# Optimization experiments

Measured on AMD Instinct MI355X. Metric: run time of the kernel, lower is better.

## Reference

```python
import jax, jax.numpy as jnp
import numpy as np

N_HEAD = 16
N_FEAT = 1024
D_K = N_FEAT // N_HEAD


def setup_inputs() -> dict:
    key = jax.random.key(0)
    ks = jax.random.split(key, 11)
    B, T1, T2 = 2, 2048, 2048
    s = 0.02
    return {
        "query": jax.random.normal(ks[0], (B, T1, N_FEAT), jnp.float32),
        "key_": jax.random.normal(ks[1], (B, T2, N_FEAT), jnp.float32),
        "value": jax.random.normal(ks[2], (B, T2, N_FEAT), jnp.float32),
        "mask": jnp.ones((B, T1, T2), jnp.int32),
        "Wq": jax.random.normal(ks[3], (N_FEAT, N_FEAT), jnp.float32) * s,
        "bq": jnp.zeros((N_FEAT,), jnp.float32),
        "Wk": jax.random.normal(ks[4], (N_FEAT, N_FEAT), jnp.float32) * s,
        "bk": jnp.zeros((N_FEAT,), jnp.float32),
        "Wv": jax.random.normal(ks[5], (N_FEAT, N_FEAT), jnp.float32) * s,
        "bv": jnp.zeros((N_FEAT,), jnp.float32),
        "Wo": jax.random.normal(ks[6], (N_FEAT, N_FEAT), jnp.float32) * s,
        "bo": jnp.zeros((N_FEAT,), jnp.float32),
    }


def reference(query, key_, value, mask, Wq, bq, Wk, bk, Wv, bv, Wo, bo):
    B = query.shape[0]
    # project and split heads: (B, T, F) -> (B, H, T, d_k)
    def heads(x, W, b):
        y = x @ W + b
        return y.reshape(B, -1, N_HEAD, D_K).transpose(0, 2, 1, 3)

    q = heads(query, Wq, bq)
    k = heads(key_, Wk, bk)
    v = heads(value, Wv, bv)

    scale = jnp.sqrt(jnp.asarray(D_K, jnp.float32))
    scores = jnp.einsum("bhqd,bhkd->bhqk", q, k) / scale  # (B,H,T1,T2)
    m = mask[:, None, :, :]  # (B,1,T1,T2)
    scores = jnp.where(m > 0, scores, jnp.asarray(-10000.0, scores.dtype))
    attn = jax.nn.softmax(scores, axis=-1)
    # dropout_rate = 0.0 / inference -> identity
    x = jnp.einsum("bhqk,bhkd->bhqd", attn, v)
    x = x.transpose(0, 2, 1, 3).reshape(B, -1, N_FEAT)
    return x @ Wo + bo
```

## Files before the change

### kernel.cpp

```cpp
#include <hip/hip_runtime.h>
#include <hip/hip_bf16.h>
#include <stdint.h>

typedef float  f32x4 __attribute__((ext_vector_type(4)));
typedef short  s16x8 __attribute__((ext_vector_type(8)));
typedef short  s16x4 __attribute__((ext_vector_type(4)));
typedef int    i32x4 __attribute__((ext_vector_type(4)));

#define DI __device__ __forceinline__

constexpr int Bb = 2, Tt = 2048, Ff = 1024, Hh = 16, Dk = 64;
constexpr int Mm = Bb * Tt;
constexpr float LOG2E = 1.44269504088896340736f;

DI ushort f2bf(float f) {
  unsigned u = __float_as_uint(f);
  unsigned r = (u + 0x7fffu + ((u >> 16) & 1u)) >> 16;
  return (ushort)r;
}

DI int cvt_pk_bf16(float lo, float hi) {
  __hip_bfloat162 t = __float22bfloat162_rn(make_float2(lo, hi));
  int w;
  __builtin_memcpy(&w, &t, 4);
  return w;
}

DI void gload16(const void* g, void* l) {
  __builtin_amdgcn_global_load_lds(
      (__attribute__((address_space(1))) void*)g,
      (__attribute__((address_space(3))) void*)l, 16, 0, 0);
}

__global__ __launch_bounds__(256) void cvt3_kernel(const float* __restrict__ s0, const float* __restrict__ s1,
                                                   const float* __restrict__ s2, ushort* __restrict__ d0,
                                                   ushort* __restrict__ d1, ushort* __restrict__ d2, int n8) {
  const float* src = blockIdx.y == 0 ? s0 : (blockIdx.y == 1 ? s1 : s2);
  ushort* dst = blockIdx.y == 0 ? d0 : (blockIdx.y == 1 ? d1 : d2);
  int i = blockIdx.x * 256 + threadIdx.x;
  if (i >= n8) return;
  const float4* s4 = (const float4*)src + (size_t)i * 2;
  float4 a = s4[0], b = s4[1];
  s16x8 o;
  o[0] = (short)f2bf(a.x); o[1] = (short)f2bf(a.y); o[2] = (short)f2bf(a.z); o[3] = (short)f2bf(a.w);
  o[4] = (short)f2bf(b.x); o[5] = (short)f2bf(b.y); o[6] = (short)f2bf(b.z); o[7] = (short)f2bf(b.w);
  *((s16x8*)dst + i) = o;
}

__global__ __launch_bounds__(256) void wtrans_kernel(const float* __restrict__ W0, const float* __restrict__ W1,
                                                     const float* __restrict__ W2, const float* __restrict__ W3,
                                                     ushort* __restrict__ Wt0, ushort* __restrict__ Wt1,
                                                     ushort* __restrict__ Wt2, ushort* __restrict__ Wt3) {
  const float* W; ushort* Wt;
  switch (blockIdx.z) {
    case 0: W = W0; Wt = Wt0; break;
    case 1: W = W1; Wt = Wt1; break;
    case 2: W = W2; Wt = Wt2; break;
    default: W = W3; Wt = Wt3; break;
  }
  __shared__ float tile[64][65];
  int k0 = blockIdx.y * 64, n0 = blockIdx.x * 64;
  int t = threadIdx.x, r = t >> 4, c4 = (t & 15) * 4;
#pragma unroll
  for (int i = 0; i < 4; i++) {
    int row = r + i * 16;
    const float4 v = *(const float4*)(W + (size_t)(k0 + row) * Ff + n0 + c4);
    tile[row][c4] = v.x; tile[row][c4 + 1] = v.y; tile[row][c4 + 2] = v.z; tile[row][c4 + 3] = v.w;
  }
  __syncthreads();
#pragma unroll
  for (int i = 0; i < 4; i++) {
    int n = r + i * 16;
    s16x4 o;
#pragma unroll
    for (int j = 0; j < 4; j++) o[j] = (short)f2bf(tile[c4 + j][n]);
    *(s16x4*)(Wt + (size_t)(n0 + n) * Ff + k0 + c4) = o;
  }
}

__global__ __launch_bounds__(256) void maskflag_kernel(const int* __restrict__ mask, int* __restrict__ flags) {
  int kb = blockIdx.x, qb = blockIdx.y, b = blockIdx.z;
  int t = threadIdx.x;
  __shared__ int s;
  if (t == 0) s = 1;
  __syncthreads();
  int ok = 1;
#pragma unroll
  for (int i = 0; i < 4; i++) {
    int row = qb * 64 + (t >> 4) + i * 16;
    const int4 v = *(const int4*)(mask + ((size_t)b * Tt + row) * Tt + kb * 64 + (t & 15) * 4);
    ok &= (v.x > 0) & (v.y > 0) & (v.z > 0) & (v.w > 0);
  }
  atomicAnd(&s, ok);
  __syncthreads();
  if (t == 0) flags[(b * 32 + qb) * 32 + kb] = s;
}

DI void gemm_core(const ushort* __restrict__ A, const ushort* __restrict__ Bt,
                  const float* __restrict__ bias, void* __restrict__ Cout, float scale, int mode,
                  int m0, int n0) {
  __shared__ ushort Ads[2][128 * 64];
  __shared__ ushort Bds[2][128 * 64];
  const int tid = threadIdx.x, lane = tid & 63, w = tid >> 6;
  const int wr = w >> 1, wc = w & 1;
  const int g = lane >> 4, ln = lane & 15;
  const int srow = lane >> 3;
  const int swzch = ((lane & 7) ^ srow) * 8;

  f32x4 acc[4][4];
#pragma unroll
  for (int m = 0; m < 4; m++)
#pragma unroll
    for (int n = 0; n < 4; n++) acc[m][n] = (f32x4){0.f, 0.f, 0.f, 0.f};

#pragma unroll
  for (int it = 0; it < 4; ++it) {
    const int row = w * 32 + it * 8;
    gload16(A + (size_t)(m0 + row + srow) * Ff + swzch, Ads[0] + row * 64);
    gload16(Bt + (size_t)(n0 + row + srow) * Ff + swzch, Bds[0] + row * 64);
  }
  __syncthreads();

  for (int kk = 0; kk < 16; ++kk) {
    const int cur = kk & 1;
    const int k0 = kk * 64;
    if (kk < 15) {
#pragma unroll
      for (int it = 0; it < 4; ++it) {
        const int row = w * 32 + it * 8;
        gload16(A + (size_t)(m0 + row + srow) * Ff + k0 + 64 + swzch, Ads[cur ^ 1] + row * 64);
        gload16(Bt + (size_t)(n0 + row + srow) * Ff + k0 + 64 + swzch, Bds[cur ^ 1] + row * 64);
      }
    }
    s16x8 af[4][2], bf[4][2];
#pragma unroll
    for (int m = 0; m < 4; m++)
#pragma unroll
      for (int c = 0; c < 2; c++) {
        const int ra = wr * 64 + m * 16 + ln;
        const int off = (c * 64 + g * 16) ^ ((ra & 7) << 4);
        af[m][c] = *(const s16x8*)((const char*)(Ads[cur]) + ra * 128 + off);
      }
#pragma unroll
    for (int n = 0; n < 4; n++)
#pragma unroll
      for (int c = 0; c < 2; c++) {
        const int rb = wc * 64 + n * 16 + ln;
        const int off = (c * 64 + g * 16) ^ ((rb & 7) << 4);
        bf[n][c] = *(const s16x8*)((const char*)(Bds[cur]) + rb * 128 + off);
      }
#pragma unroll
    for (int m = 0; m < 4; m++)
#pragma unroll
      for (int n = 0; n < 4; n++)
#pragma unroll
        for (int c = 0; c < 2; c++)
          acc[m][n] = __builtin_amdgcn_mfma_f32_16x16x32_bf16(af[m][c], bf[n][c], acc[m][n], 0, 0, 0);
    if (kk < 15) __syncthreads();
  }
#pragma unroll
  for (int m = 0; m < 4; m++) {
    const int r0 = m0 + wr * 64 + m * 16 + g * 4;
#pragma unroll
    for (int n = 0; n < 4; n++) {
      const int col = n0 + wc * 64 + n * 16 + ln;
      const float bv = bias[col];
      if (mode == 2) {
        const int bb = r0 >> 11, rb = r0 & 2047;
        const int x = rb & 63;
        const int pbase = (x & 0x20) | ((x & 0x0C) << 1) | ((x & 0x10) >> 2);
        s16x4 o4;
#pragma unroll
        for (int r = 0; r < 4; r++) o4[r] = (short)f2bf(acc[m][n][r] + bv);
        *(s16x4*)((ushort*)Cout + ((size_t)bb * Ff + col) * Tt + (rb & ~63) + pbase) = o4;
      } else {
#pragma unroll
        for (int r = 0; r < 4; r++) {
          const float val = (acc[m][n][r] + bv) * scale;
          if (mode == 1)
            ((ushort*)Cout)[(size_t)(r0 + r) * Ff + col] = f2bf(val);
          else
            ((float*)Cout)[(size_t)(r0 + r) * Ff + col] = val;
        }
      }
    }
  }
}

__global__ __launch_bounds__(256) void qkv_gemm_kernel(
    const ushort* __restrict__ Xq, const ushort* __restrict__ Xk, const ushort* __restrict__ Xv,
    const ushort* __restrict__ Wqt, const ushort* __restrict__ Wkt, const ushort* __restrict__ Wvt,
    const float* __restrict__ bq, const float* __restrict__ bk, const float* __restrict__ bv,
    ushort* __restrict__ Qb, ushort* __restrict__ Kb, ushort* __restrict__ Vpt) {
  const int lin = blockIdx.x + 8 * blockIdx.y + 256 * blockIdx.z;
  const int work = (lin & 7) * 96 + (lin >> 3);
  const int z = work >> 8;
  const int r = work & 255;
  const int m0 = (r >> 3) * 128, n0 = (r & 7) * 128;
  const ushort* A = z == 0 ? Xq : (z == 1 ? Xk : Xv);
  const ushort* Wt = z == 0 ? Wqt : (z == 1 ? Wkt : Wvt);
  const float* bias = z == 0 ? bq : (z == 1 ? bk : bv);
  void* C = z == 0 ? (void*)Qb : (z == 1 ? (void*)Kb : (void*)Vpt);
  const float scale = z == 0 ? 0.125f * LOG2E : 1.0f;
  gemm_core(A, Wt, bias, C, scale, z == 2 ? 2 : 1, m0, n0);
}

__global__ __launch_bounds__(256) void out_gemm_kernel(const ushort* __restrict__ AO,
                                                       const ushort* __restrict__ Wot,
                                                       const float* __restrict__ bo,
                                                       float* __restrict__ Out) {
  const int lin = blockIdx.x + 8 * blockIdx.y;
  const int work = (lin & 7) * 32 + (lin >> 3);
  const int m0 = (work >> 3) * 128, n0 = (work & 7) * 128;
  gemm_core(AO, Wot, bo, Out, 1.0f, 0, m0, n0);
}

__global__ __launch_bounds__(256) void flash_kernel(
    const ushort* __restrict__ Qb, const ushort* __restrict__ Kb, const ushort* __restrict__ Vpt,
    const int* __restrict__ flags, const int* __restrict__ mask, ushort* __restrict__ AO) {
  __shared__ ushort Ks[2][64 * 64];
  __shared__ ushort Vs[2][64 * 64];
  const int lin = blockIdx.x + 16 * (blockIdx.y + 16 * blockIdx.z);
  const int work = (lin & 7) * 64 + (lin >> 3);
  const int qb = work & 15, h = (work >> 4) & 15, b = work >> 8;
  const int tid = threadIdx.x, lane = tid & 63, w = tid >> 6;
  const int g = lane >> 4, ln = lane & 15;

  const ushort* Qg = Qb + ((size_t)b * Tt + qb * 128) * Ff + h * Dk;
  const ushort* Kg = Kb + ((size_t)b * Tt) * Ff + h * Dk;
  const ushort* Vg = Vpt + (size_t)(b * Ff + h * Dk) * Tt;

  const int srow = lane >> 3;
  const int swzch = ((lane & 7) ^ srow) * 8;

#pragma unroll
  for (int it = 0; it < 2; ++it) {
    const int row = w * 16 + it * 8;
    gload16(Kg + (size_t)(row + srow) * Ff + swzch, Ks[0] + row * 64);
    gload16(Vg + (size_t)(row + srow) * Tt + swzch, Vs[0] + row * 64);
  }
  const int* flagrow0 = flags + (b * 32 + qb * 2) * 32;
  const int f0 = (lane < 32) ? flagrow0[lane] : 1;
  const int f1 = (lane < 32) ? flagrow0[32 + lane] : 1;

  s16x8 qf0[2], qf1[2];
  {
    const ushort* Qrow0 = Qg + (size_t)(w * 16 + ln) * Ff;
    const ushort* Qrow1 = Qrow0 + (size_t)64 * Ff;
    qf0[0] = *(const s16x8*)(Qrow0 + g * 8);
    qf0[1] = *(const s16x8*)(Qrow0 + 32 + g * 8);
    qf1[0] = *(const s16x8*)(Qrow1 + g * 8);
    qf1[1] = *(const s16x8*)(Qrow1 + 32 + g * 8);
  }
  __syncthreads();
  const unsigned long long bm0 = __ballot(f0 == 0);
  const unsigned long long bm1 = __ballot(f1 == 0);

  float l0 = 0.f, l1 = 0.f;
  f32x4 o0[4], o1[4];
#pragma unroll
  for (int ds = 0; ds < 4; ds++) { o0[ds] = (f32x4){0.f, 0.f, 0.f, 0.f}; o1[ds] = (f32x4){0.f, 0.f, 0.f, 0.f}; }

  auto body = [&](const ushort* Kc, const ushort* Vc, ushort* Kn, ushort* Vn, int kt) {
    if (kt + 1 < 32) {
      const ushort* Kg2 = Kg + (size_t)(kt + 1) * 64 * Ff;
      const ushort* Vg2 = Vg + (size_t)(kt + 1) * 64;
#pragma unroll
      for (int it = 0; it < 2; ++it) {
        const int row = w * 16 + it * 8;
        gload16(Kg2 + (size_t)(row + srow) * Ff + swzch, Kn + row * 64);
        gload16(Vg2 + (size_t)(row + srow) * Tt + swzch, Vn + row * 64);
      }
    }
    f32x4 sf0[4], sf1[4];
    __builtin_amdgcn_s_setprio(1);
#pragma unroll
    for (int ks = 0; ks < 4; ++ks) {
      f32x4 a0 = (f32x4){0.f, 0.f, 0.f, 0.f};
      f32x4 a1 = (f32x4){0.f, 0.f, 0.f, 0.f};
#pragma unroll
      for (int c = 0; c < 2; c++) {
        const int row = ks * 16 + ln;
        const int off = (c * 64 + g * 16) ^ ((row & 7) << 4);
        const s16x8 kf = *(const s16x8*)((const char*)Kc + row * 128 + off);
        a0 = __builtin_amdgcn_mfma_f32_16x16x32_bf16(kf, qf0[c], a0, 0, 0, 0);
        a1 = __builtin_amdgcn_mfma_f32_16x16x32_bf16(kf, qf1[c], a1, 0, 0, 0);
      }
      sf0[ks] = a0; sf1[ks] = a1;
    }
    __builtin_amdgcn_s_setprio(0);
    if ((bm0 >> kt) & 1ull) {
      const int qg_ = qb * 128 + w * 16 + ln;
#pragma unroll
      for (int ks = 0; ks < 4; ++ks) {
        const int4 mv = *(const int4*)(mask + ((size_t)b * Tt + qg_) * Tt + kt * 64 + ks * 16 + g * 4);
        if (mv.x <= 0) sf0[ks][0] = -10000.f;
        if (mv.y <= 0) sf0[ks][1] = -10000.f;
        if (mv.z <= 0) sf0[ks][2] = -10000.f;
        if (mv.w <= 0) sf0[ks][3] = -10000.f;
      }
    }
    if ((bm1 >> kt) & 1ull) {
      const int qg_ = qb * 128 + 64 + w * 16 + ln;
#pragma unroll
      for (int ks = 0; ks < 4; ++ks) {
        const int4 mv = *(const int4*)(mask + ((size_t)b * Tt + qg_) * Tt + kt * 64 + ks * 16 + g * 4);
        if (mv.x <= 0) sf1[ks][0] = -10000.f;
        if (mv.y <= 0) sf1[ks][1] = -10000.f;
        if (mv.z <= 0) sf1[ks][2] = -10000.f;
        if (mv.w <= 0) sf1[ks][3] = -10000.f;
      }
    }
    float a0 = 0.f, a1 = 0.f;
#pragma unroll
    for (int ks = 0; ks < 4; ++ks) {
#pragma unroll
      for (int r = 0; r < 4; ++r) {
        const float p0 = __builtin_amdgcn_exp2f(sf0[ks][r]);
        const float p1 = __builtin_amdgcn_exp2f(sf1[ks][r]);
        sf0[ks][r] = p0; sf1[ks][r] = p1;
        a0 += p0; a1 += p1;
      }
    }
    l0 += a0; l1 += a1;
    i32x4 paw0[2], paw1[2];
#pragma unroll
    for (int c = 0; c < 2; c++)
#pragma unroll
      for (int f = 0; f < 2; f++)
#pragma unroll
        for (int hh = 0; hh < 2; hh++) {
          paw0[c][f * 2 + hh] = cvt_pk_bf16(sf0[2 * c + f][2 * hh], sf0[2 * c + f][2 * hh + 1]);
          paw1[c][f * 2 + hh] = cvt_pk_bf16(sf1[2 * c + f][2 * hh], sf1[2 * c + f][2 * hh + 1]);
        }
    const s16x8 pa00 = __builtin_bit_cast(s16x8, paw0[0]);
    const s16x8 pa01 = __builtin_bit_cast(s16x8, paw0[1]);
    const s16x8 pa10 = __builtin_bit_cast(s16x8, paw1[0]);
    const s16x8 pa11 = __builtin_bit_cast(s16x8, paw1[1]);
    __builtin_amdgcn_s_setprio(1);
#pragma unroll
    for (int ds = 0; ds < 4; ++ds) {
      const int row = ds * 16 + ln;
#pragma unroll
      for (int c = 0; c < 2; ++c) {
        const int off = (c * 64 + g * 16) ^ ((row & 7) << 4);
        const s16x8 vf = *(const s16x8*)((const char*)Vc + row * 128 + off);
        o0[ds] = __builtin_amdgcn_mfma_f32_16x16x32_bf16(c == 0 ? pa00 : pa01, vf, o0[ds], 0, 0, 0);
        o1[ds] = __builtin_amdgcn_mfma_f32_16x16x32_bf16(c == 0 ? pa10 : pa11, vf, o1[ds], 0, 0, 0);
      }
    }
    __builtin_amdgcn_s_setprio(0);
    __syncthreads();
  };

  for (int kt = 0; kt < 32; kt += 2) {
    body(Ks[0], Vs[0], Ks[1], Vs[1], kt);
    body(Ks[1], Vs[1], Ks[0], Vs[0], kt + 1);
  }

  l0 += __shfl_xor(l0, 16); l0 += __shfl_xor(l0, 32);
  l1 += __shfl_xor(l1, 16); l1 += __shfl_xor(l1, 32);
  float inv0[4], inv1[4];
#pragma unroll
  for (int r = 0; r < 4; ++r) {
    inv0[r] = 1.0f / __shfl(l0, g * 4 + r);
    inv1[r] = 1.0f / __shfl(l1, g * 4 + r);
  }
  ushort* AOg0 = AO + ((size_t)b * Tt + qb * 128 + w * 16) * Ff + h * Dk;
  ushort* AOg1 = AOg0 + (size_t)64 * Ff;
#pragma unroll
  for (int ds = 0; ds < 4; ++ds)
#pragma unroll
    for (int r = 0; r < 4; ++r) {
      AOg0[(size_t)(g * 4 + r) * Ff + ds * 16 + ln] = f2bf(o0[ds][r] * inv0[r]);
      AOg1[(size_t)(g * 4 + r) * Ff + ds * 16 + ln] = f2bf(o1[ds][r] * inv1[r]);
    }
}

extern "C" void kernel_launch(void* const* d_in, const int* in_sizes, int n_in,
                              void* d_out, int out_size, void* d_ws, size_t ws_size,
                              hipStream_t stream) {
  const float* query = (const float*)d_in[0];
  const float* key_  = (const float*)d_in[1];
  const float* value = (const float*)d_in[2];
  const int*   mask  = (const int*)d_in[3];
  const float* Wq = (const float*)d_in[4];  const float* bq = (const float*)d_in[5];
  const float* Wk = (const float*)d_in[6];  const float* bk = (const float*)d_in[7];
  const float* Wv = (const float*)d_in[8];  const float* bv = (const float*)d_in[9];
  const float* Wo = (const float*)d_in[10]; const float* bo = (const float*)d_in[11];
  float* Out = (float*)d_out;

  constexpr size_t SZ_X = (size_t)Mm * Ff * 2;
  constexpr size_t SZ_W = (size_t)Ff * Ff * 2;
  uintptr_t p = (uintptr_t)d_ws;
  auto alloc = [&](size_t sz) { void* r = (void*)p; p += (sz + 255) & ~(size_t)255; return r; };
  ushort* Xq = (ushort*)alloc(SZ_X);
  ushort* Xk = (ushort*)alloc(SZ_X);
  ushort* Xv = (ushort*)alloc(SZ_X);
  ushort* Wqt = (ushort*)alloc(SZ_W);
  ushort* Wkt = (ushort*)alloc(SZ_W);
  ushort* Wvt = (ushort*)alloc(SZ_W);
  ushort* Wot = (ushort*)alloc(SZ_W);
  ushort* Qp  = (ushort*)alloc(SZ_X);
  ushort* Kp  = (ushort*)alloc(SZ_X);
  ushort* Vpt = (ushort*)alloc(SZ_X);
  int* flags = (int*)alloc((size_t)Bb * 32 * 32 * 4);
  ushort* AO = Xq;

  const int n8 = Mm * Ff / 8;
  cvt3_kernel<<<dim3(2048, 3), 256, 0, stream>>>(query, key_, value, Xq, Xk, Xv, n8);
  wtrans_kernel<<<dim3(16, 16, 4), 256, 0, stream>>>(Wq, Wk, Wv, Wo, Wqt, Wkt, Wvt, Wot);
  maskflag_kernel<<<dim3(32, 32, 2), 256, 0, stream>>>(mask, flags);
  qkv_gemm_kernel<<<dim3(8, 32, 3), 256, 0, stream>>>(Xq, Xk, Xv, Wqt, Wkt, Wvt, bq, bk, bv, Qp, Kp, Vpt);
  flash_kernel<<<dim3(16, 16, 2), 256, 0, stream>>>(Qp, Kp, Vpt, flags, mask, AO);
  out_gemm_kernel<<<dim3(8, 32), 256, 0, stream>>>(AO, Wot, bo, Out);
}
```

Before: 145.6 us.

## Use triple-buffered LDS pipelines with vmcnt waits in GEMM and flash kernels

Both the projection GEMM and the flash-attention kernel move from double-buffered LDS with a full __syncthreads per iteration to three-slot ring buffers. Tiles are prefetched two iterations ahead, and each iteration waits with s_waitcnt vmcnt(4) plus a single s_barrier. The GEMM also halves its K-step to 32 and drops the XOR swizzle in favour of a plain row layout. The aim is to hide global-load latency and cut barrier stalls. In exchange it uses more LDS (which may lower occupancy), risks LDS bank conflicts from the unswizzled layout, and depends on exact vmcnt bookkeeping, which may not account for the flag and Q loads.

Measured after the change: 144.0 us. About the same (-1.1%).

```diff
diff --git a/kernel.cpp b/kernel.cpp
--- a/kernel.cpp
+++ b/kernel.cpp
@@ -31,6 +31,9 @@
       (__attribute__((address_space(1))) void*)g,
       (__attribute__((address_space(3))) void*)l, 16, 0, 0);
 }
+
+DI void wait_vm4() { asm volatile("s_waitcnt vmcnt(4)" ::: "memory"); }
+DI void wait_vm0() { asm volatile("s_waitcnt vmcnt(0)" ::: "memory"); }
 
 __global__ __launch_bounds__(256) void cvt3_kernel(const float* __restrict__ s0, const float* __restrict__ s1,
                                                    const float* __restrict__ s2, ushort* __restrict__ d0,
@@ -99,13 +102,20 @@
 DI void gemm_core(const ushort* __restrict__ A, const ushort* __restrict__ Bt,
                   const float* __restrict__ bias, void* __restrict__ Cout, float scale, int mode,
                   int m0, int n0) {
-  __shared__ ushort Ads[2][128 * 64];
-  __shared__ ushort Bds[2][128 * 64];
+  __shared__ ushort Ads[3][128 * 32];
+  __shared__ ushort Bds[3][128 * 32];
   const int tid = threadIdx.x, lane = tid & 63, w = tid >> 6;
   const int wr = w >> 1, wc = w & 1;
   const int g = lane >> 4, ln = lane & 15;
-  const int srow = lane >> 3;
-  const int swzch = ((lane & 7) ^ srow) * 8;
+  const int strow = tid >> 2;
+  const int stc = (tid & 3) * 8;
+
+  const ushort* Asrc0 = A + (size_t)(m0 + strow) * Ff + stc;
+  const ushort* Asrc1 = A + (size_t)(m0 + 64 + strow) * Ff + stc;
+  const ushort* Bsrc0 = Bt + (size_t)(n0 + strow) * Ff + stc;
+  const ushort* Bsrc1 = Bt + (size_t)(n0 + 64 + strow) * Ff + stc;
+  const int dst0 = strow * 32 + stc;
+  const int dst1 = (64 + strow) * 32 + stc;
 
   f32x4 acc[4][4];
 #pragma unroll
@@ -113,50 +123,39 @@
 #pragma unroll
     for (int n = 0; n < 4; n++) acc[m][n] = (f32x4){0.f, 0.f, 0.f, 0.f};
 
-#pragma unroll
-  for (int it = 0; it < 4; ++it) {
-    const int row = w * 32 + it * 8;
-    gload16(A + (size_t)(m0 + row + srow) * Ff + swzch, Ads[0] + row * 64);
-    gload16(Bt + (size_t)(n0 + row + srow) * Ff + swzch, Bds[0] + row * 64);
-  }
-  __syncthreads();
-
-  for (int kk = 0; kk < 16; ++kk) {
-    const int cur = kk & 1;
-    const int k0 = kk * 64;
-    if (kk < 15) {
-#pragma unroll
-      for (int it = 0; it < 4; ++it) {
-        const int row = w * 32 + it * 8;
-        gload16(A + (size_t)(m0 + row + srow) * Ff + k0 + 64 + swzch, Ads[cur ^ 1] + row * 64);
-        gload16(Bt + (size_t)(n0 + row + srow) * Ff + k0 + 64 + swzch, Bds[cur ^ 1] + row * 64);
-      }
-    }
-    s16x8 af[4][2], bf[4][2];
+  auto stage = [&](int t, int slot) {
+    const int k0 = t * 32;
+    gload16(Asrc0 + k0, Ads[slot] + dst0);
+    gload16(Asrc1 + k0, Ads[slot] + dst1);
+    gload16(Bsrc0 + k0, Bds[slot] + dst0);
+    gload16(Bsrc1 + k0, Bds[slot] + dst1);
+  };
+
+  stage(0, 0);
+  stage(1, 1);
+
+  int rs = 0, ws = 2;
+  for (int t = 0; t < 32; ++t) {
+    if (t < 31) wait_vm4(); else wait_vm0();
+    __builtin_amdgcn_s_barrier();
+    __builtin_amdgcn_sched_barrier(0);
+    if (t < 30) stage(t + 2, ws);
+    const ushort* As = Ads[rs];
+    const ushort* Bs = Bds[rs];
+    s16x8 af[4], bf[4];
+#pragma unroll
+    for (int m = 0; m < 4; m++) af[m] = *(const s16x8*)(As + (wr * 64 + m * 16 + ln) * 32 + g * 8);
+#pragma unroll
+    for (int n = 0; n < 4; n++) bf[n] = *(const s16x8*)(Bs + (wc * 64 + n * 16 + ln) * 32 + g * 8);
+    __builtin_amdgcn_s_setprio(1);
 #pragma unroll
     for (int m = 0; m < 4; m++)
 #pragma unroll
-      for (int c = 0; c < 2; c++) {
-        const int ra = wr * 64 + m * 16 + ln;
-        const int off = (c * 64 + g * 16) ^ ((ra & 7) << 4);
-        af[m][c] = *(const s16x8*)((const char*)(Ads[cur]) + ra * 128 + off);
-      }
-#pragma unroll
-    for (int n = 0; n < 4; n++)
-#pragma unroll
-      for (int c = 0; c < 2; c++) {
-        const int rb = wc * 64 + n * 16 + ln;
-        const int off = (c * 64 + g * 16) ^ ((rb & 7) << 4);
-        bf[n][c] = *(const s16x8*)((const char*)(Bds[cur]) + rb * 128 + off);
-      }
-#pragma unroll
-    for (int m = 0; m < 4; m++)
-#pragma unroll
       for (int n = 0; n < 4; n++)
-#pragma unroll
-        for (int c = 0; c < 2; c++)
-          acc[m][n] = __builtin_amdgcn_mfma_f32_16x16x32_bf16(af[m][c], bf[n][c], acc[m][n], 0, 0, 0);
-    if (kk < 15) __syncthreads();
+        acc[m][n] = __builtin_amdgcn_mfma_f32_16x16x32_bf16(af[m], bf[n], acc[m][n], 0, 0, 0);
+    __builtin_amdgcn_s_setprio(0);
+    rs = rs == 2 ? 0 : rs + 1;
+    ws = ws == 2 ? 0 : ws + 1;
   }
 #pragma unroll
   for (int m = 0; m < 4; m++) {
@@ -218,8 +217,8 @@
 __global__ __launch_bounds__(256) void flash_kernel(
     const ushort* __restrict__ Qb, const ushort* __restrict__ Kb, const ushort* __restrict__ Vpt,
     const int* __restrict__ flags, const int* __restrict__ mask, ushort* __restrict__ AO) {
-  __shared__ ushort Ks[2][64 * 64];
-  __shared__ ushort Vs[2][64 * 64];
+  __shared__ ushort Ks[3][64 * 64];
+  __shared__ ushort Vs[3][64 * 64];
   const int lin = blockIdx.x + 16 * (blockIdx.y + 16 * blockIdx.z);
   const int work = (lin & 7) * 64 + (lin >> 3);
   const int qb = work & 15, h = (work >> 4) & 15, b = work >> 8;
@@ -232,16 +231,6 @@
 
   const int srow = lane >> 3;
   const int swzch = ((lane & 7) ^ srow) * 8;
-
-#pragma unroll
-  for (int it = 0; it < 2; ++it) {
-    const int row = w * 16 + it * 8;
-    gload16(Kg + (size_t)(row + srow) * Ff + swzch, Ks[0] + row * 64);
-    gload16(Vg + (size_t)(row + srow) * Tt + swzch, Vs[0] + row * 64);
-  }
-  const int* flagrow0 = flags + (b * 32 + qb * 2) * 32;
-  const int f0 = (lane < 32) ? flagrow0[lane] : 1;
-  const int f1 = (lane < 32) ? flagrow0[32 + lane] : 1;
 
   s16x8 qf0[2], qf1[2];
   {
@@ -252,7 +241,22 @@
     qf1[0] = *(const s16x8*)(Qrow1 + g * 8);
     qf1[1] = *(const s16x8*)(Qrow1 + 32 + g * 8);
   }
-  __syncthreads();
+  const int* flagrow0 = flags + (b * 32 + qb * 2) * 32;
+  const int f0 = (lane < 32) ? flagrow0[lane] : 1;
+  const int f1 = (lane < 32) ? flagrow0[32 + lane] : 1;
+
+  auto stage = [&](int t, int slot) {
+    const ushort* Kg2 = Kg + (size_t)t * 64 * Ff;
+    const ushort* Vg2 = Vg + (size_t)t * 64;
+#pragma unroll
+    for (int it = 0; it < 2; ++it) {
+      const int row = w * 16 + it * 8;
+      gload16(Kg2 + (size_t)(row + srow) * Ff + swzch, Ks[slot] + row * 64);
+      gload16(Vg2 + (size_t)(row + srow) * Tt + swzch, Vs[slot] + row * 64);
+    }
+  };
+  stage(0, 0);
+  stage(1, 1);
   const unsigned long long bm0 = __ballot(f0 == 0);
   const unsigned long long bm1 = __ballot(f1 == 0);
 
@@ -261,17 +265,14 @@
 #pragma unroll
   for (int ds = 0; ds < 4; ds++) { o0[ds] = (f32x4){0.f, 0.f, 0.f, 0.f}; o1[ds] = (f32x4){0.f, 0.f, 0.f, 0.f}; }
 
-  auto body = [&](const ushort* Kc, const ushort* Vc, ushort* Kn, ushort* Vn, int kt) {
-    if (kt + 1 < 32) {
-      const ushort* Kg2 = Kg + (size_t)(kt + 1) * 64 * Ff;
-      const ushort* Vg2 = Vg + (size_t)(kt + 1) * 64;
-#pragma unroll
-      for (int it = 0; it < 2; ++it) {
-        const int row = w * 16 + it * 8;
-        gload16(Kg2 + (size_t)(row + srow) * Ff + swzch, Kn + row * 64);
-        gload16(Vg2 + (size_t)(row + srow) * Tt + swzch, Vn + row * 64);
-      }
-    }
+  int rs = 0, ws = 2;
+  for (int kt = 0; kt < 32; ++kt) {
+    if (kt < 31) wait_vm4(); else wait_vm0();
+    __builtin_amdgcn_s_barrier();
+    __builtin_amdgcn_sched_barrier(0);
+    if (kt < 30) stage(kt + 2, ws);
+    const ushort* Kc = Ks[rs];
+    const ushort* Vc = Vs[rs];
     f32x4 sf0[4], sf1[4];
     __builtin_amdgcn_s_setprio(1);
 #pragma unroll
@@ -350,12 +351,8 @@
       }
     }
     __builtin_amdgcn_s_setprio(0);
-    __syncthreads();
-  };
-
-  for (int kt = 0; kt < 32; kt += 2) {
-    body(Ks[0], Vs[0], Ks[1], Vs[1], kt);
-    body(Ks[1], Vs[1], Ks[0], Vs[0], kt + 1);
+    rs = rs == 2 ? 0 : rs + 1;
+    ws = ws == 2 ? 0 : ws + 1;
   }
 
   l0 += __shfl_xor(l0, 16); l0 += __shfl_xor(l0, 32);
```
